# Optimization experiments

Measured on AMD Instinct MI355X. Metric: run time of the kernel, lower is better.

Reference implementation:

```python
import jax, jax.numpy as jnp
import numpy as np

N_DST = 100_000
N_SRC = 200_000
DEG = 16            # fixed avg degree -> E = N_DST*DEG
E = N_DST * DEG
P, K, W = 16, 256, 8  # num_parts, codebook entries, part width; feat_dim = P*W = 128
F_IN = P * W
F_OUT = 128


def setup_inputs() -> dict:
    key = jax.random.key(0)
    k1, k2, k3, k4, k5, k6, k7 = jax.random.split(key, 7)
    codes = jax.random.randint(k1, (N_SRC, P), 0, K, dtype=jnp.int32)
    indices = jax.random.randint(k2, (E,), 0, N_SRC, dtype=jnp.int32)
    indptr = (jnp.arange(N_DST + 1, dtype=jnp.int32) * DEG)
    h_self = jax.random.normal(k3, (N_DST, F_IN), dtype=jnp.float32)
    codebook = jax.random.normal(k4, (P, K, W), dtype=jnp.float32)
    W_neigh = jax.random.normal(k5, (F_OUT, F_IN), dtype=jnp.float32) * (1.0 / np.sqrt(F_IN))
    W_self = jax.random.normal(k6, (F_OUT, F_IN), dtype=jnp.float32) * (1.0 / np.sqrt(F_IN))
    b_self = jax.random.normal(k7, (F_OUT,), dtype=jnp.float32) * 0.01
    return {"codes": codes, "indices": indices, "indptr": indptr, "h_self": h_self,
            "codebook": codebook, "W_neigh": W_neigh, "W_self": W_self, "b_self": b_self}


def reference(codes, indices, indptr, h_self, codebook, W_neigh, W_self, b_self):
    n_dst = indptr.shape[0] - 1
    n_edges = indices.shape[0]
    # --- VQ decompress: codebook[p, codes[n, p]] -> [N_src, P, W] -> [N_src, F_IN]
    feat = codebook[jnp.arange(P)[None, :], codes]          # [N_src, P, W]
    feat = feat.reshape(feat.shape[0], F_IN)                # [N_src, F_IN]
    # --- CSR(CSC) mean SpMM over neighbors
    # dst id of each edge from indptr (jit-safe, static E)
    dst_ids = jnp.searchsorted(indptr, jnp.arange(n_edges, dtype=indptr.dtype), side="right") - 1
    gathered = feat[indices]                                 # [E, F_IN] (irregular gather)
    summed = jax.ops.segment_sum(gathered, dst_ids, num_segments=n_dst)  # [N_dst, F_IN]
    deg = jnp.diff(indptr).astype(summed.dtype)
    h_neigh = summed / jnp.maximum(deg, 1.0)[:, None]        # mean aggregation
    # --- linear combine: fc_neigh(h_neigh) + fc_self(h_self)
    rst = h_neigh @ W_neigh.T + h_self @ W_self.T + b_self[None, :]
    return rst
```

## Files before the change

### kernel.cpp

```cpp
#include <hip/hip_runtime.h>
#include <stdint.h>

constexpr int N_DST = 100000;
constexpr int N_SRC = 200000;
constexpr int DEG   = 16;
constexpr int PP    = 16;
constexpr int KK    = 256;
constexpr int WW    = 8;
constexpr int F_IN  = 128;
constexpr int F_OUT = 128;

typedef __attribute__((ext_vector_type(8))) short short8;
typedef __attribute__((ext_vector_type(4))) float floatx4;

__device__ __forceinline__ unsigned short f2bf(float f) {
    unsigned int u = __float_as_uint(f);
    unsigned int r = (u + 0x7FFFu + ((u >> 16) & 1u)) >> 16;
    return (unsigned short)r;
}
__device__ __forceinline__ float bf2f(unsigned int bits16) {
    return __uint_as_float(bits16 << 16);
}

constexpr int DT = 64;
constexpr int NT = (N_DST + DT - 1) / DT;
constexpr int LDS_STRIDE = 264;

__global__ __launch_bounds__(1024, 1) void fused_kernel(
    const int* __restrict__ codes, const int* __restrict__ indices,
    const float* __restrict__ codebook, const float* __restrict__ h_self,
    const float* __restrict__ Wn, const float* __restrict__ Ws,
    const float* __restrict__ b_self, float* __restrict__ out)
{
    __shared__ __align__(16) unsigned short scb[KK * PP * WW];
    __shared__ __align__(16) unsigned short hcat[2][DT][LDS_STRIDE];

    const int tid  = threadIdx.x;
    const int wv   = tid >> 6;
    const int lane = tid & 63;
    const int quad = lane >> 4;
    const int r    = lane & 15;
    const int p    = lane & 15;
    const int sub  = lane >> 4;

    {
        const float4* cb4 = (const float4*)codebook;
        ushort4* s4 = (ushort4*)scb;
        #pragma unroll
        for (int it = 0; it < 8; ++it) {
            const int i = tid + it * 1024;
            const float4 v = cb4[i];
            const int pp   = i >> 9;
            const int k    = (i >> 1) & 255;
            const int half = i & 1;
            ushort4 w;
            w.x = f2bf(v.x); w.y = f2bf(v.y); w.z = f2bf(v.z); w.w = f2bf(v.w);
            s4[((k << 4) | pp) * 2 + half] = w;
        }
    }

    const int cg = wv & 7;
    const int rg = wv >> 3;
    short8 bfrag[8];
    #pragma unroll
    for (int kt = 0; kt < 8; ++kt) {
        const int o  = cg * 16 + r;
        const int kb = kt * 32 + quad * 8;
        const float* src = (kb < 128) ? (Wn + o * 128 + kb)
                                      : (Ws + o * 128 + (kb - 128));
        union { short8 v; unsigned short u[8]; } f;
        #pragma unroll
        for (int j = 0; j < 8; ++j) f.u[j] = f2bf(src[j]);
        bfrag[kt] = f.v;
    }
    const float bs = b_self[cg * 16 + r];

    __syncthreads();

    const int G = gridDim.x;
    int buf = 0;
    for (int t = blockIdx.x; t < NT; t += G) {
        const int d0 = t * DT;

        const int dbase = d0 + wv * 4;
        int sidx = 0;
        if (dbase + sub < N_DST) sidx = indices[dbase * DEG + lane];

        const int hrow = tid >> 4;
        const int hcol = tid & 15;
        const int hd   = d0 + hrow;
        float4 ha = make_float4(0.f, 0.f, 0.f, 0.f);
        float4 hb = ha;
        if (hd < N_DST) {
            const float4* s4 = (const float4*)(h_self + (size_t)hd * F_IN + hcol * 8);
            ha = s4[0]; hb = s4[1];
        }

        int c[16];
        #pragma unroll
        for (int e = 0; e < 16; ++e) {
            const int s = __shfl(sidx, (lane & 48) | e, 64);
            c[e] = codes[s * PP + p];
        }

        float ga[8];
        #pragma unroll
        for (int i = 0; i < 8; ++i) ga[i] = 0.f;
        #pragma unroll
        for (int e = 0; e < 16; ++e) {
            const uint4 q = *(const uint4*)(scb + (((c[e] << 4) | p) << 3));
            ga[0] += bf2f(q.x & 0xFFFFu);
            ga[1] += bf2f(q.x >> 16);
            ga[2] += bf2f(q.y & 0xFFFFu);
            ga[3] += bf2f(q.y >> 16);
            ga[4] += bf2f(q.z & 0xFFFFu);
            ga[5] += bf2f(q.z >> 16);
            ga[6] += bf2f(q.w & 0xFFFFu);
            ga[7] += bf2f(q.w >> 16);
        }

        {
            uint4 o4;
            o4.x = (unsigned int)f2bf(ga[0] * 0.0625f) | ((unsigned int)f2bf(ga[1] * 0.0625f) << 16);
            o4.y = (unsigned int)f2bf(ga[2] * 0.0625f) | ((unsigned int)f2bf(ga[3] * 0.0625f) << 16);
            o4.z = (unsigned int)f2bf(ga[4] * 0.0625f) | ((unsigned int)f2bf(ga[5] * 0.0625f) << 16);
            o4.w = (unsigned int)f2bf(ga[6] * 0.0625f) | ((unsigned int)f2bf(ga[7] * 0.0625f) << 16);
            *(uint4*)&hcat[buf][wv * 4 + sub][p * 8] = o4;
        }

        {
            uint4 hw;
            hw.x = (unsigned int)f2bf(ha.x) | ((unsigned int)f2bf(ha.y) << 16);
            hw.y = (unsigned int)f2bf(ha.z) | ((unsigned int)f2bf(ha.w) << 16);
            hw.z = (unsigned int)f2bf(hb.x) | ((unsigned int)f2bf(hb.y) << 16);
            hw.w = (unsigned int)f2bf(hb.z) | ((unsigned int)f2bf(hb.w) << 16);
            *(uint4*)&hcat[buf][hrow][128 + hcol * 8] = hw;
        }

        __syncthreads();

        floatx4 acc0 = (floatx4)(0.f);
        floatx4 acc1 = (floatx4)(0.f);
        #pragma unroll
        for (int kt = 0; kt < 8; ++kt) {
            const short8 a0 = *(const short8*)&hcat[buf][rg * 32 + r][kt * 32 + quad * 8];
            const short8 a1 = *(const short8*)&hcat[buf][rg * 32 + 16 + r][kt * 32 + quad * 8];
            acc0 = __builtin_amdgcn_mfma_f32_16x16x32_bf16(a0, bfrag[kt], acc0, 0, 0, 0);
            acc1 = __builtin_amdgcn_mfma_f32_16x16x32_bf16(a1, bfrag[kt], acc1, 0, 0, 0);
        }

        #pragma unroll
        for (int e = 0; e < 4; ++e) {
            const int d = d0 + rg * 32 + quad * 4 + e;
            if (d < N_DST) out[(size_t)d * F_OUT + cg * 16 + r] = acc0[e] + bs;
        }
        #pragma unroll
        for (int e = 0; e < 4; ++e) {
            const int d = d0 + rg * 32 + 16 + quad * 4 + e;
            if (d < N_DST) out[(size_t)d * F_OUT + cg * 16 + r] = acc1[e] + bs;
        }

        buf ^= 1;
    }
}

extern "C" void kernel_launch(void* const* d_in, const int* in_sizes, int n_in,
                              void* d_out, int out_size, void* d_ws, size_t ws_size,
                              hipStream_t stream) {
    const int*   codes    = (const int*)d_in[0];
    const int*   indices  = (const int*)d_in[1];
    const float* h_self   = (const float*)d_in[3];
    const float* codebook = (const float*)d_in[4];
    const float* W_neigh  = (const float*)d_in[5];
    const float* W_self   = (const float*)d_in[6];
    const float* b_self   = (const float*)d_in[7];
    float*       out      = (float*)d_out;

    fused_kernel<<<256, 1024, 0, stream>>>(codes, indices, codebook, h_self,
                                           W_neigh, W_self, b_self, out);
}
```

Baseline: 161.4 us.

## Split fused kernel into separate gather and GEMM kernels via workspace

Replaces the single fused gather+GEMM kernel with two kernels. A gather kernel decodes and averages neighbor codebook rows into a bf16 buffer in workspace. A GEMM kernel then reads that buffer plus h_self, with weights staged in XOR-swizzled LDS. The split frees the gather phase from the fused kernel's one-block-per-CU occupancy limit. In exchange it adds an intermediate write and read of about 25MB plus a second launch. The fused kernel remains as a fallback when the workspace is too small.

```diff
diff --git a/kernel.cpp b/kernel.cpp
--- a/kernel.cpp
+++ b/kernel.cpp
@@ -18,8 +18,164 @@
     unsigned int r = (u + 0x7FFFu + ((u >> 16) & 1u)) >> 16;
     return (unsigned short)r;
 }
-__device__ __forceinline__ float bf2f(unsigned int bits16) {
-    return __uint_as_float(bits16 << 16);
+__device__ __forceinline__ float bf_lo(unsigned int q) {
+    return __uint_as_float(q << 16);
+}
+__device__ __forceinline__ float bf_hi(unsigned int q) {
+    return __uint_as_float(q & 0xFFFF0000u);
+}
+
+
+__global__ __launch_bounds__(1024, 8) void gather_kernel(
+    const int* __restrict__ codes, const int* __restrict__ indices,
+    const float* __restrict__ codebook, unsigned short* __restrict__ hn)
+{
+    __shared__ __align__(16) unsigned short scb[KK * PP * WW];
+
+    const int tid = threadIdx.x;
+
+    {
+        const float4* cb4 = (const float4*)codebook;
+        ushort4* s4 = (ushort4*)scb;
+        #pragma unroll
+        for (int it = 0; it < 8; ++it) {
+            const int i = tid + it * 1024;
+            const float4 v = cb4[i];
+            const int pp   = i >> 9;
+            const int k    = (i >> 1) & 255;
+            const int half = i & 1;
+            ushort4 w;
+            w.x = f2bf(v.x); w.y = f2bf(v.y); w.z = f2bf(v.z); w.w = f2bf(v.w);
+            s4[((k << 4) | pp) * 2 + half] = w;
+        }
+    }
+    __syncthreads();
+
+    const int wv   = tid >> 6;
+    const int lane = tid & 63;
+    const int p    = lane & 15;
+    const int sub  = lane >> 4;
+
+    const int gw0 = blockIdx.x * 16 + wv;
+    const int NW  = gridDim.x * 16;
+    for (int g = gw0; g < N_DST / 4; g += NW) {
+        const int dbase = g * 4;
+
+        const int sidx = indices[dbase * DEG + lane];
+
+        int c[16];
+        #pragma unroll
+        for (int e = 0; e < 16; ++e) {
+            const int s = __shfl(sidx, (lane & 48) | e, 64);
+            c[e] = codes[s * PP + p];
+        }
+
+        float ga[8];
+        #pragma unroll
+        for (int i = 0; i < 8; ++i) ga[i] = 0.f;
+        #pragma unroll
+        for (int e = 0; e < 16; ++e) {
+            const uint4 q = *(const uint4*)(scb + (((c[e] << 4) | p) << 3));
+            ga[0] += bf_lo(q.x); ga[1] += bf_hi(q.x);
+            ga[2] += bf_lo(q.y); ga[3] += bf_hi(q.y);
+            ga[4] += bf_lo(q.z); ga[5] += bf_hi(q.z);
+            ga[6] += bf_lo(q.w); ga[7] += bf_hi(q.w);
+        }
+
+        uint4 o4;
+        o4.x = (unsigned int)f2bf(ga[0] * 0.0625f) | ((unsigned int)f2bf(ga[1] * 0.0625f) << 16);
+        o4.y = (unsigned int)f2bf(ga[2] * 0.0625f) | ((unsigned int)f2bf(ga[3] * 0.0625f) << 16);
+        o4.z = (unsigned int)f2bf(ga[4] * 0.0625f) | ((unsigned int)f2bf(ga[5] * 0.0625f) << 16);
+        o4.w = (unsigned int)f2bf(ga[6] * 0.0625f) | ((unsigned int)f2bf(ga[7] * 0.0625f) << 16);
+        *(uint4*)&hn[(size_t)(dbase + sub) * 128 + p * 8] = o4;
+    }
+}
+
+constexpr int RT2 = 64;
+constexpr int NT2 = (N_DST + RT2 - 1) / RT2;
+
+__global__ __launch_bounds__(512, 4) void gemm_kernel(
+    const unsigned short* __restrict__ hn, const float* __restrict__ h_self,
+    const float* __restrict__ Wn, const float* __restrict__ Ws,
+    const float* __restrict__ b_self, float* __restrict__ out)
+{
+    __shared__ __align__(16) unsigned short wlds[F_OUT][256];
+
+    const int tid  = threadIdx.x;
+    const int wv   = tid >> 6;
+    const int lane = tid & 63;
+    const int quad = lane >> 4;
+    const int r    = lane & 15;
+
+    #pragma unroll
+    for (int j = 0; j < 16; ++j) {
+        const int fi = tid + j * 512;
+        const int o  = fi >> 6;
+        const int fc = fi & 63;
+        const int k  = fc * 4;
+        const float* src = (k < 128) ? (Wn + o * 128 + k)
+                                     : (Ws + o * 128 + (k - 128));
+        const float4 v = *(const float4*)src;
+        ushort4 w;
+        w.x = f2bf(v.x); w.y = f2bf(v.y); w.z = f2bf(v.z); w.w = f2bf(v.w);
+        const int ch = fc >> 1;
+        const int hc = fc & 1;
+        *(ushort4*)&wlds[o][((ch ^ (o & 7)) << 3) + hc * 4] = w;
+    }
+    __syncthreads();
+
+    const int rt = wv & 3;
+    const int co = (wv >> 2) * 64;
+    float bsv[4];
+    #pragma unroll
+    for (int n = 0; n < 4; ++n) bsv[n] = b_self[co + n * 16 + r];
+
+    for (int t = blockIdx.x; t < NT2; t += gridDim.x) {
+        const int d0   = t * RT2;
+        const int drow = d0 + rt * 16 + r;
+
+        floatx4 acc[4];
+        #pragma unroll
+        for (int n = 0; n < 4; ++n) acc[n] = (floatx4)(0.f);
+
+        #pragma unroll
+        for (int kt = 0; kt < 8; ++kt) {
+            short8 a;
+            if (kt < 4) {
+                a = *(const short8*)&hn[(size_t)drow * 128 + kt * 32 + quad * 8];
+            } else {
+                float4 xa = make_float4(0.f, 0.f, 0.f, 0.f);
+                float4 xb = xa;
+                if (drow < N_DST) {
+                    const float4* s4 = (const float4*)(h_self + (size_t)drow * 128
+                                                       + (kt - 4) * 32 + quad * 8);
+                    xa = s4[0]; xb = s4[1];
+                }
+                union { short8 v; unsigned short u[8]; } f;
+                f.u[0] = f2bf(xa.x); f.u[1] = f2bf(xa.y);
+                f.u[2] = f2bf(xa.z); f.u[3] = f2bf(xa.w);
+                f.u[4] = f2bf(xb.x); f.u[5] = f2bf(xb.y);
+                f.u[6] = f2bf(xb.z); f.u[7] = f2bf(xb.w);
+                a = f.v;
+            }
+            #pragma unroll
+            for (int n = 0; n < 4; ++n) {
+                const int o = co + n * 16 + r;
+                const short8 b = *(const short8*)
+                    &wlds[o][(((kt * 4 + quad) ^ (o & 7)) << 3)];
+                acc[n] = __builtin_amdgcn_mfma_f32_16x16x32_bf16(a, b, acc[n], 0, 0, 0);
+            }
+        }
+
+        #pragma unroll
+        for (int n = 0; n < 4; ++n) {
+            #pragma unroll
+            for (int e = 0; e < 4; ++e) {
+                const int d = d0 + rt * 16 + quad * 4 + e;
+                if (d < N_DST) out[(size_t)d * F_OUT + co + n * 16 + r] = acc[n][e] + bsv[n];
+            }
+        }
+    }
 }
 
 constexpr int DT = 64;
@@ -81,7 +237,6 @@
     int buf = 0;
     for (int t = blockIdx.x; t < NT; t += G) {
         const int d0 = t * DT;
-
         const int dbase = d0 + wv * 4;
         int sidx = 0;
         if (dbase + sub < N_DST) sidx = indices[dbase * DEG + lane];
@@ -109,14 +264,10 @@
         #pragma unroll
         for (int e = 0; e < 16; ++e) {
             const uint4 q = *(const uint4*)(scb + (((c[e] << 4) | p) << 3));
-            ga[0] += bf2f(q.x & 0xFFFFu);
-            ga[1] += bf2f(q.x >> 16);
-            ga[2] += bf2f(q.y & 0xFFFFu);
-            ga[3] += bf2f(q.y >> 16);
-            ga[4] += bf2f(q.z & 0xFFFFu);
-            ga[5] += bf2f(q.z >> 16);
-            ga[6] += bf2f(q.w & 0xFFFFu);
-            ga[7] += bf2f(q.w >> 16);
+            ga[0] += bf_lo(q.x); ga[1] += bf_hi(q.x);
+            ga[2] += bf_lo(q.y); ga[3] += bf_hi(q.y);
+            ga[4] += bf_lo(q.z); ga[5] += bf_hi(q.z);
+            ga[6] += bf_lo(q.w); ga[7] += bf_hi(q.w);
         }
 
         {
@@ -127,7 +278,6 @@
             o4.w = (unsigned int)f2bf(ga[6] * 0.0625f) | ((unsigned int)f2bf(ga[7] * 0.0625f) << 16);
             *(uint4*)&hcat[buf][wv * 4 + sub][p * 8] = o4;
         }
-
         {
             uint4 hw;
             hw.x = (unsigned int)f2bf(ha.x) | ((unsigned int)f2bf(ha.y) << 16);
@@ -176,6 +326,13 @@
     const float* b_self   = (const float*)d_in[7];
     float*       out      = (float*)d_out;
 
-    fused_kernel<<<256, 1024, 0, stream>>>(codes, indices, codebook, h_self,
-                                           W_neigh, W_self, b_self, out);
-}
+    const size_t need = (size_t)NT2 * RT2 * 128 * sizeof(unsigned short);
+    if (d_ws != nullptr && ws_size >= need) {
+        unsigned short* hn = (unsigned short*)d_ws;
+        gather_kernel<<<512, 1024, 0, stream>>>(codes, indices, codebook, hn);
+        gemm_kernel<<<512, 512, 0, stream>>>(hn, h_self, W_neigh, W_self, b_self, out);
+    } else {
+        fused_kernel<<<256, 1024, 0, stream>>>(codes, indices, codebook, h_self,
+                                               W_neigh, W_self, b_self, out);
+    }
+}
```

Result: slower. 213.3 us (+32.2%).

## Prefetch next tile's indices, codes and self features across loop iterations

Applied to the files above, without the earlier changes.

Software-pipelines the persistent tile loop: the next tile's edge indices, codebook codes and h_self rows are loaded while the current tile's gather-accumulate and MFMA run, hiding global memory latency. It also replaces the high-half bf16 unpack with a mask and raises the launch bound's minimum blocks per CU. The extra live registers for prefetched data, together with the tighter register cap implied by the launch bound, risk register spilling.

```diff
diff --git a/kernel.cpp b/kernel.cpp
--- a/kernel.cpp
+++ b/kernel.cpp
@@ -18,15 +18,18 @@
     unsigned int r = (u + 0x7FFFu + ((u >> 16) & 1u)) >> 16;
     return (unsigned short)r;
 }
-__device__ __forceinline__ float bf2f(unsigned int bits16) {
-    return __uint_as_float(bits16 << 16);
+__device__ __forceinline__ float bf_lo(unsigned int q) {
+    return __uint_as_float(q << 16);
+}
+__device__ __forceinline__ float bf_hi(unsigned int q) {
+    return __uint_as_float(q & 0xFFFF0000u);
 }
 
 constexpr int DT = 64;
 constexpr int NT = (N_DST + DT - 1) / DT;
 constexpr int LDS_STRIDE = 264;
 
-__global__ __launch_bounds__(1024, 1) void fused_kernel(
+__global__ __launch_bounds__(1024, 4) void fused_kernel(
     const int* __restrict__ codes, const int* __restrict__ indices,
     const float* __restrict__ codebook, const float* __restrict__ h_self,
     const float* __restrict__ Wn, const float* __restrict__ Ws,
@@ -78,46 +81,69 @@
     __syncthreads();
 
     const int G = gridDim.x;
-    int buf = 0;
-    for (int t = blockIdx.x; t < NT; t += G) {
-        const int d0 = t * DT;
-
-        const int dbase = d0 + wv * 4;
+    const int hrow = tid >> 4;
+    const int hcol = tid & 15;
+
+    int t = blockIdx.x;
+    int c_cur[16];
+    float4 ha_c = make_float4(0.f, 0.f, 0.f, 0.f);
+    float4 hb_c = ha_c;
+    {
+        const int dbase = t * DT + wv * 4;
         int sidx = 0;
         if (dbase + sub < N_DST) sidx = indices[dbase * DEG + lane];
-
-        const int hrow = tid >> 4;
-        const int hcol = tid & 15;
-        const int hd   = d0 + hrow;
-        float4 ha = make_float4(0.f, 0.f, 0.f, 0.f);
-        float4 hb = ha;
+        const int hd = t * DT + hrow;
         if (hd < N_DST) {
             const float4* s4 = (const float4*)(h_self + (size_t)hd * F_IN + hcol * 8);
-            ha = s4[0]; hb = s4[1];
-        }
-
-        int c[16];
+            ha_c = s4[0]; hb_c = s4[1];
+        }
         #pragma unroll
         for (int e = 0; e < 16; ++e) {
             const int s = __shfl(sidx, (lane & 48) | e, 64);
-            c[e] = codes[s * PP + p];
-        }
+            c_cur[e] = codes[s * PP + p];
+        }
+    }
+
+    int buf = 0;
+    for (; t < NT; t += G) {
+        const int d0 = t * DT;
+        const int tn = t + G;
+
+        int sidx_n = 0;
+        {
+            const int dbase = tn * DT + wv * 4;
+            if (dbase + sub < N_DST) sidx_n = indices[dbase * DEG + lane];
+        }
+        float4 ha_n = make_float4(0.f, 0.f, 0.f, 0.f);
+        float4 hb_n = ha_n;
+        {
+            const int hd = tn * DT + hrow;
+            if (hd < N_DST) {
+                const float4* s4 = (const float4*)(h_self + (size_t)hd * F_IN + hcol * 8);
+                ha_n = s4[0]; hb_n = s4[1];
+            }
+        }
+        __builtin_amdgcn_sched_barrier(0);
 
         float ga[8];
         #pragma unroll
         for (int i = 0; i < 8; ++i) ga[i] = 0.f;
         #pragma unroll
         for (int e = 0; e < 16; ++e) {
-            const uint4 q = *(const uint4*)(scb + (((c[e] << 4) | p) << 3));
-            ga[0] += bf2f(q.x & 0xFFFFu);
-            ga[1] += bf2f(q.x >> 16);
-            ga[2] += bf2f(q.y & 0xFFFFu);
-            ga[3] += bf2f(q.y >> 16);
-            ga[4] += bf2f(q.z & 0xFFFFu);
-            ga[5] += bf2f(q.z >> 16);
-            ga[6] += bf2f(q.w & 0xFFFFu);
-            ga[7] += bf2f(q.w >> 16);
-        }
+            const uint4 q = *(const uint4*)(scb + (((c_cur[e] << 4) | p) << 3));
+            ga[0] += bf_lo(q.x); ga[1] += bf_hi(q.x);
+            ga[2] += bf_lo(q.y); ga[3] += bf_hi(q.y);
+            ga[4] += bf_lo(q.z); ga[5] += bf_hi(q.z);
+            ga[6] += bf_lo(q.w); ga[7] += bf_hi(q.w);
+        }
+
+        int c_nxt[16];
+        #pragma unroll
+        for (int e = 0; e < 16; ++e) {
+            const int s = __shfl(sidx_n, (lane & 48) | e, 64);
+            c_nxt[e] = codes[s * PP + p];
+        }
+        __builtin_amdgcn_sched_barrier(0);
 
         {
             uint4 o4;
@@ -127,13 +153,12 @@
             o4.w = (unsigned int)f2bf(ga[6] * 0.0625f) | ((unsigned int)f2bf(ga[7] * 0.0625f) << 16);
             *(uint4*)&hcat[buf][wv * 4 + sub][p * 8] = o4;
         }
-
         {
             uint4 hw;
-            hw.x = (unsigned int)f2bf(ha.x) | ((unsigned int)f2bf(ha.y) << 16);
-            hw.y = (unsigned int)f2bf(ha.z) | ((unsigned int)f2bf(ha.w) << 16);
-            hw.z = (unsigned int)f2bf(hb.x) | ((unsigned int)f2bf(hb.y) << 16);
-            hw.w = (unsigned int)f2bf(hb.z) | ((unsigned int)f2bf(hb.w) << 16);
+            hw.x = (unsigned int)f2bf(ha_c.x) | ((unsigned int)f2bf(ha_c.y) << 16);
+            hw.y = (unsigned int)f2bf(ha_c.z) | ((unsigned int)f2bf(ha_c.w) << 16);
+            hw.z = (unsigned int)f2bf(hb_c.x) | ((unsigned int)f2bf(hb_c.y) << 16);
+            hw.w = (unsigned int)f2bf(hb_c.z) | ((unsigned int)f2bf(hb_c.w) << 16);
             *(uint4*)&hcat[buf][hrow][128 + hcol * 8] = hw;
         }
 
@@ -160,6 +185,9 @@
             if (d < N_DST) out[(size_t)d * F_OUT + cg * 16 + r] = acc1[e] + bs;
         }
 
+        #pragma unroll
+        for (int e = 0; e < 16; ++e) c_cur[e] = c_nxt[e];
+        ha_c = ha_n; hb_c = hb_n;
         buf ^= 1;
     }
 }
```

After: 209.8 us. 30.0% more time.
